# Optimization experiments

Hardware: AMD Instinct MI355X
Metric: run time of the kernel (lower is better)

## Reference

```python
import jax, jax.numpy as jnp
import numpy as np

INF = 1e20


def setup_inputs() -> dict:
    key = jax.random.key(0)
    k1, k2, k3 = jax.random.split(key, 3)
    B, Q, M, F, D = 16, 64, 512, 16, 512
    return {
        "query_embed": jax.random.normal(k1, (B, Q, D), dtype=jnp.float32),
        "in_memory_embed": jax.random.normal(k2, (B, M, F, D), dtype=jnp.float32),
        "out_memory_embed": jax.random.normal(k3, (B, M, F, D), dtype=jnp.float32),
        "ctx_mask": jnp.ones((B, M, F), dtype=jnp.float32),
        "query_mask": jnp.ones((B, Q), dtype=jnp.float32),
    }


def reference(query_embed, in_memory_embed, out_memory_embed, ctx_mask, query_mask):
    # co-attention scores: [B, Q, M, F]
    attention = jnp.einsum("bqd,bmfd->bqmf", query_embed, in_memory_embed)
    # additive INF masking (torch: mask*att - (1-mask)*INF)
    cm = ctx_mask[:, None, :, :]            # [B,1,M,F]
    attention = cm * attention - (1.0 - cm) * INF
    qm = query_mask[:, :, None, None]       # [B,Q,1,1]
    attention = qm * attention - (1.0 - qm) * INF
    # NOTE: torch code computes a max-pool over Q for kb_feature_att but
    # immediately overwrites it with softmax of a ones/ctx mask -> dead code.
    mask = ctx_mask * 1.0 - (1.0 - ctx_mask) * INF        # [B,M,F]
    kb_feature_att = jax.nn.softmax(mask, axis=-1)        # [B,M,F]
    # weighted read over feature slots: [B,M,D]
    in_mem = jnp.einsum("bmf,bmfd->bmd", kb_feature_att, in_memory_embed)
    out_mem = out_memory_embed.sum(axis=2)                # [B,M,D]
    # max-pool over feature axis F -> [B,Q,M]
    att_qm = attention.max(axis=-1)
    probs = jax.nn.softmax(att_qm, axis=-1)               # over M
    new_query_embed = query_embed + jnp.einsum("bqm,bmd->bqd", probs, out_mem)
    probs2 = jax.nn.softmax(att_qm, axis=1)               # over Q
    in_mem = in_mem + jnp.einsum("bqm,bqd->bmd", probs2, new_query_embed)
    return (new_query_embed, in_mem, out_mem)
```

## Files before the change

kernel.cpp:

```cpp
#include <hip/hip_runtime.h>

#define INF_F 1e20f
#define B_ 16
#define Q_ 64
#define M_ 512
#define F_ 16
#define D_ 512

typedef __attribute__((ext_vector_type(8))) short short8v;
typedef __attribute__((ext_vector_type(4))) float f32x4;

static __device__ __forceinline__ float bits_f(unsigned int u) { return __uint_as_float(u); }
static __device__ __forceinline__ float lo_f(unsigned int u) { return __uint_as_float(u << 16); }
static __device__ __forceinline__ float hi_f(unsigned int u) { return __uint_as_float(u & 0xffff0000u); }

static __device__ __forceinline__ int lds_off(int row, int gran) {
    return row * 40 + ((gran ^ (row & 3)) << 3);
}

static __device__ __forceinline__ void conv_store(short* __restrict__ Hb, short* __restrict__ Lb,
                                                  int row, int c, float4 v) {
    unsigned ux = __float_as_uint(v.x), uy = __float_as_uint(v.y);
    unsigned uz = __float_as_uint(v.z), uw = __float_as_uint(v.w);
    unsigned hx = ux & 0xffff0000u, hy = uy & 0xffff0000u;
    unsigned hz = uz & 0xffff0000u, hw = uw & 0xffff0000u;
    float lx = v.x - bits_f(hx), ly = v.y - bits_f(hy);
    float lz = v.z - bits_f(hz), lw = v.w - bits_f(hw);
    uint2 H, L;
    H.x = (hx >> 16) | hy;
    H.y = (hz >> 16) | hw;
    L.x = (__float_as_uint(lx) >> 16) | (__float_as_uint(ly) & 0xffff0000u);
    L.y = (__float_as_uint(lz) >> 16) | (__float_as_uint(lw) & 0xffff0000u);
    int off = row * 40 + (((c >> 1) ^ (row & 3)) << 3) + ((c & 1) << 2);
    *(uint2*)&Hb[off] = H;
    *(uint2*)&Lb[off] = L;
}

__global__ __launch_bounds__(256) void k_att_mfma(
    const float* __restrict__ query, const float* __restrict__ in_mem,
    const float* __restrict__ ctx_mask, const float* __restrict__ query_mask,
    float* __restrict__ att_qm, float* __restrict__ in_mem_base)
{
    __shared__ __align__(16) short Qh[2][64 * 40];
    __shared__ __align__(16) short Ql[2][64 * 40];
    __shared__ __align__(16) short Mh[2][64 * 40];
    __shared__ __align__(16) short Ml[2][64 * 40];

    const int bid = blockIdx.x;
    const int b   = bid & 15;
    const int m0  = (bid >> 4) * 4;
    const int t   = threadIdx.x;
    const int w   = t >> 6;
    const int lane = t & 63;
    const int lr  = lane & 15;
    const int lg  = lane >> 4;
    const int c8  = lane & 7;
    const int fg  = lane >> 3;

    float w_lo, w_hi;
    {
        const float* cm = ctx_mask + ((size_t)b * M_ + m0 + w) * F_;
        float wv[F_]; float mx = -INF_F;
        #pragma unroll
        for (int f = 0; f < F_; ++f) {
            float cv = cm[f];
            float v = cv - (1.0f - cv) * INF_F;
            wv[f] = v; mx = fmaxf(mx, v);
        }
        float s = 0.f;
        #pragma unroll
        for (int f = 0; f < F_; ++f) { wv[f] = __expf(wv[f] - mx); s += wv[f]; }
        float inv = 1.0f / s;
        w_lo = wv[fg] * inv; w_hi = wv[fg + 8] * inv;
    }

    const float4* q4 = (const float4*)query;
    const float4* m4 = (const float4*)in_mem;
    const size_t qbase = (size_t)b * Q_ * 128;
    const size_t mbase = ((size_t)b * M_ + m0) * F_ * 128;
    const int srow0 = t >> 3, scol = t & 7;
    const int srow1 = srow0 + 32;

    f32x4 acc[4];
    #pragma unroll
    for (int j = 0; j < 4; ++j) acc[j] = (f32x4){0, 0, 0, 0};

    float4 qA[2], mA[2], qB[2], mB[2];

#define LOAD_CHUNK(qd, md, kc) do { int k4 = (kc) * 8;                           \
        qd[0] = q4[qbase + (size_t)srow0 * 128 + k4 + scol];                     \
        qd[1] = q4[qbase + (size_t)srow1 * 128 + k4 + scol];                     \
        md[0] = m4[mbase + (size_t)srow0 * 128 + k4 + scol];                     \
        md[1] = m4[mbase + (size_t)srow1 * 128 + k4 + scol]; } while (0)

#define CONV_CHUNK(qd, md, bi) do {                                              \
        conv_store(Qh[bi], Ql[bi], srow0, scol, qd[0]);                          \
        conv_store(Qh[bi], Ql[bi], srow1, scol, qd[1]);                          \
        conv_store(Mh[bi], Ml[bi], srow0, scol, md[0]);                          \
        conv_store(Mh[bi], Ml[bi], srow1, scol, md[1]); } while (0)

#define MFMA_FSUM(bi, kc) do {                                                   \
        short8v bh = *(const short8v*)&Mh[bi][lds_off(w * 16 + lr, lg)];         \
        short8v bl = *(const short8v*)&Ml[bi][lds_off(w * 16 + lr, lg)];         \
        _Pragma("unroll")                                                        \
        for (int tq = 0; tq < 4; ++tq) {                                         \
            short8v ah = *(const short8v*)&Qh[bi][lds_off(tq * 16 + lr, lg)];    \
            short8v al = *(const short8v*)&Ql[bi][lds_off(tq * 16 + lr, lg)];    \
            acc[tq] = __builtin_amdgcn_mfma_f32_16x16x32_bf16(ah, bh, acc[tq], 0, 0, 0); \
            acc[tq] = __builtin_amdgcn_mfma_f32_16x16x32_bf16(ah, bl, acc[tq], 0, 0, 0); \
            acc[tq] = __builtin_amdgcn_mfma_f32_16x16x32_bf16(al, bh, acc[tq], 0, 0, 0); \
        }                                                                        \
        float4 s = make_float4(0, 0, 0, 0);                                      \
        {   int rr = w * 16 + fg;                                                \
            int off = rr * 40 + (((c8 >> 1) ^ (rr & 3)) << 3) + ((c8 & 1) << 2); \
            uint2 H = *(const uint2*)&Mh[bi][off];                               \
            uint2 L = *(const uint2*)&Ml[bi][off];                               \
            s.x += w_lo * (lo_f(H.x) + lo_f(L.x));                               \
            s.y += w_lo * (hi_f(H.x) + hi_f(L.x));                               \
            s.z += w_lo * (lo_f(H.y) + lo_f(L.y));                               \
            s.w += w_lo * (hi_f(H.y) + hi_f(L.y));                               \
        }                                                                        \
        {   int rr = w * 16 + fg + 8;                                            \
            int off = rr * 40 + (((c8 >> 1) ^ (rr & 3)) << 3) + ((c8 & 1) << 2); \
            uint2 H = *(const uint2*)&Mh[bi][off];                               \
            uint2 L = *(const uint2*)&Ml[bi][off];                               \
            s.x += w_hi * (lo_f(H.x) + lo_f(L.x));                               \
            s.y += w_hi * (hi_f(H.x) + hi_f(L.x));                               \
            s.z += w_hi * (lo_f(H.y) + lo_f(L.y));                               \
            s.w += w_hi * (hi_f(H.y) + hi_f(L.y));                               \
        }                                                                        \
        _Pragma("unroll")                                                        \
        for (int sh = 8; sh <= 32; sh <<= 1) {                                   \
            s.x += __shfl_xor(s.x, sh, 64); s.y += __shfl_xor(s.y, sh, 64);      \
            s.z += __shfl_xor(s.z, sh, 64); s.w += __shfl_xor(s.w, sh, 64);      \
        }                                                                        \
        if (fg == 0)                                                             \
            ((float4*)in_mem_base)[((size_t)b * M_ + m0 + w) * 128 + (kc) * 8 + c8] = s; \
    } while (0)

    LOAD_CHUNK(qA, mA, 0);
    #pragma unroll
    for (int it = 0; it < 8; ++it) {
        int kc0 = 2 * it, kc1 = 2 * it + 1;
        LOAD_CHUNK(qB, mB, kc1);
        CONV_CHUNK(qA, mA, 0);
        __syncthreads();
        MFMA_FSUM(0, kc0);
        if (it < 7) LOAD_CHUNK(qA, mA, kc0 + 2);
        CONV_CHUNK(qB, mB, 1);
        __syncthreads();
        MFMA_FSUM(1, kc1);
    }

    {
        int m = m0 + w;
        float cmv = ctx_mask[((size_t)b * M_ + m) * F_ + lr];
        #pragma unroll
        for (int tq = 0; tq < 4; ++tq) {
            #pragma unroll
            for (int rg = 0; rg < 4; ++rg) {
                int q = tq * 16 + lg * 4 + rg;
                float qmv = query_mask[b * Q_ + q];
                float v = acc[tq][rg];
                v = cmv * v - (1.0f - cmv) * INF_F;
                v = qmv * v - (1.0f - qmv) * INF_F;
                #pragma unroll
                for (int sh = 1; sh < 16; sh <<= 1) v = fmaxf(v, __shfl_xor(v, sh, 64));
                if (lr == 0)
                    att_qm[((size_t)b * Q_ + q) * M_ + m] = v;
            }
        }
    }
#undef LOAD_CHUNK
#undef CONV_CHUNK
#undef MFMA_FSUM
}

__global__ __launch_bounds__(256) void k_out_sum(
    const float* __restrict__ om, float* __restrict__ os)
{
    int bm = blockIdx.x * 2 + (threadIdx.x >> 7);
    int c  = threadIdx.x & 127;
    const float4* src = (const float4*)om + (size_t)bm * F_ * 128 + c;
    float4 a = make_float4(0, 0, 0, 0);
    #pragma unroll
    for (int f = 0; f < F_; ++f) {
        float4 v = src[(size_t)f * 128];
        a.x += v.x; a.y += v.y; a.z += v.z; a.w += v.w;
    }
    ((float4*)os)[(size_t)bm * 128 + c] = a;
}

__global__ __launch_bounds__(128) void k_new_query(
    const float* __restrict__ att, const float* __restrict__ query,
    const float* __restrict__ out_sum, float* __restrict__ new_q)
{
    __shared__ float P[8][512];
    int bid = blockIdx.x;
    int b = bid & 15, qc = bid >> 4;
    int t = threadIdx.x;
    {
        int qi = t >> 4, l16 = t & 15;
        const float* row = att + ((size_t)b * Q_ + qc * 8 + qi) * M_;
        float vals[32]; float mx = -INF_F;
        #pragma unroll
        for (int i = 0; i < 32; ++i) { vals[i] = row[l16 + i * 16]; mx = fmaxf(mx, vals[i]); }
        #pragma unroll
        for (int s = 1; s < 16; s <<= 1) mx = fmaxf(mx, __shfl_xor(mx, s, 64));
        float sm = 0.f;
        #pragma unroll
        for (int i = 0; i < 32; ++i) { vals[i] = __expf(vals[i] - mx); sm += vals[i]; }
        #pragma unroll
        for (int s = 1; s < 16; s <<= 1) sm += __shfl_xor(sm, s, 64);
        float inv = 1.0f / sm;
        #pragma unroll
        for (int i = 0; i < 32; ++i) P[qi][l16 + i * 16] = vals[i] * inv;
    }
    __syncthreads();
    int c = t;
    const float4* o4 = (const float4*)out_sum + (size_t)b * M_ * 128 + c;
    const float4* q4 = (const float4*)query + ((size_t)b * Q_ + qc * 8) * 128 + c;
    float4 acc[8];
    #pragma unroll
    for (int qi = 0; qi < 8; ++qi) acc[qi] = q4[(size_t)qi * 128];
    for (int mm = 0; mm < M_; mm += 4) {
        float4 o0 = o4[(size_t)(mm + 0) * 128];
        float4 o1 = o4[(size_t)(mm + 1) * 128];
        float4 o2 = o4[(size_t)(mm + 2) * 128];
        float4 o3 = o4[(size_t)(mm + 3) * 128];
        #pragma unroll
        for (int qi = 0; qi < 8; ++qi) {
            float4 p = *(const float4*)&P[qi][mm];
            acc[qi].x += p.x * o0.x + p.y * o1.x + p.z * o2.x + p.w * o3.x;
            acc[qi].y += p.x * o0.y + p.y * o1.y + p.z * o2.y + p.w * o3.y;
            acc[qi].z += p.x * o0.z + p.y * o1.z + p.z * o2.z + p.w * o3.z;
            acc[qi].w += p.x * o0.w + p.y * o1.w + p.z * o2.w + p.w * o3.w;
        }
    }
    float4* n4 = (float4*)new_q + ((size_t)b * Q_ + qc * 8) * 128 + c;
    #pragma unroll
    for (int qi = 0; qi < 8; ++qi) n4[(size_t)qi * 128] = acc[qi];
}

__global__ __launch_bounds__(128) void k_in_mem(
    const float* __restrict__ att, const float* __restrict__ new_q,
    float* __restrict__ in_mem_io)
{
    __shared__ float P[8][64];
    int bid = blockIdx.x;
    int b = bid & 15, mc = bid >> 4;
    int m0 = mc * 8;
    int t = threadIdx.x;
    {
        int mi = t >> 4, l16 = t & 15;
        float v[4]; float mx = -INF_F;
        #pragma unroll
        for (int i = 0; i < 4; ++i) {
            v[i] = att[((size_t)b * Q_ + l16 + i * 16) * M_ + m0 + mi];
            mx = fmaxf(mx, v[i]);
        }
        #pragma unroll
        for (int s = 1; s < 16; s <<= 1) mx = fmaxf(mx, __shfl_xor(mx, s, 64));
        float sm = 0.f;
        #pragma unroll
        for (int i = 0; i < 4; ++i) { v[i] = __expf(v[i] - mx); sm += v[i]; }
        #pragma unroll
        for (int s = 1; s < 16; s <<= 1) sm += __shfl_xor(sm, s, 64);
        float inv = 1.0f / sm;
        #pragma unroll
        for (int i = 0; i < 4; ++i) P[mi][l16 + i * 16] = v[i] * inv;
    }
    __syncthreads();
    int c = t;
    float4* io = (float4*)in_mem_io + ((size_t)b * M_ + m0) * 128 + c;
    const float4* n4 = (const float4*)new_q + (size_t)b * Q_ * 128 + c;
    float4 acc[8];
    #pragma unroll
    for (int mi = 0; mi < 8; ++mi) acc[mi] = io[(size_t)mi * 128];
    for (int q = 0; q < Q_; q += 4) {
        float4 n0 = n4[(size_t)(q + 0) * 128];
        float4 n1 = n4[(size_t)(q + 1) * 128];
        float4 n2 = n4[(size_t)(q + 2) * 128];
        float4 n3 = n4[(size_t)(q + 3) * 128];
        #pragma unroll
        for (int mi = 0; mi < 8; ++mi) {
            float4 p = *(const float4*)&P[mi][q];
            acc[mi].x += p.x * n0.x + p.y * n1.x + p.z * n2.x + p.w * n3.x;
            acc[mi].y += p.x * n0.y + p.y * n1.y + p.z * n2.y + p.w * n3.y;
            acc[mi].z += p.x * n0.z + p.y * n1.z + p.z * n2.z + p.w * n3.z;
            acc[mi].w += p.x * n0.w + p.y * n1.w + p.z * n2.w + p.w * n3.w;
        }
    }
    #pragma unroll
    for (int mi = 0; mi < 8; ++mi) io[(size_t)mi * 128] = acc[mi];
}

extern "C" void kernel_launch(void* const* d_in, const int* in_sizes, int n_in,
                              void* d_out, int out_size, void* d_ws, size_t ws_size,
                              hipStream_t stream)
{
    const float* query      = (const float*)d_in[0];
    const float* in_mem     = (const float*)d_in[1];
    const float* out_mem    = (const float*)d_in[2];
    const float* ctx_mask   = (const float*)d_in[3];
    const float* query_mask = (const float*)d_in[4];

    float* out = (float*)d_out;
    float* new_q      = out;
    float* in_mem_out = out + (size_t)B_*Q_*D_;
    float* out_mem_o  = in_mem_out + (size_t)B_*M_*D_;

    float* att_qm = (float*)d_ws;

    hipLaunchKernelGGL(k_att_mfma, dim3((M_/4) * B_), dim3(256), 0, stream,
                       query, in_mem, ctx_mask, query_mask, att_qm, in_mem_out);
    hipLaunchKernelGGL(k_out_sum, dim3(B_*M_/2), dim3(256), 0, stream,
                       out_mem, out_mem_o);
    hipLaunchKernelGGL(k_new_query, dim3(8 * B_), dim3(128), 0, stream,
                       att_qm, query, out_mem_o, new_q);
    hipLaunchKernelGGL(k_in_mem, dim3(64 * B_), dim3(128), 0, stream,
                       att_qm, new_q, in_mem_out);
}
```

Measured before the change: 229.6 us.

## Fuse out-memory feature sum into attention kernel and pre-split query to bf16

The separate out_memory feature-sum kernel is folded into the main MFMA attention kernel, which now streams out_mem alongside in_mem and reduces over F with warp shuffles. The query is split into bf16 hi/lo once by a new pre-pass kernel, so each attention block no longer reconverts it and just copies the pre-split halves into LDS. The weighted in_mem read now uses the fp32 values held in registers instead of rereading the split values from LDS, and __syncthreads is replaced by an explicit lgkmcnt wait plus s_barrier. The fused kernel carries more register pressure and a larger per-block load, and there is one extra small launch.

After: 238.0 us. 1.04x slower.

```diff
diff --git a/kernel.cpp b/kernel.cpp
--- a/kernel.cpp
+++ b/kernel.cpp
@@ -11,40 +11,54 @@
 typedef __attribute__((ext_vector_type(4))) float f32x4;
 
 static __device__ __forceinline__ float bits_f(unsigned int u) { return __uint_as_float(u); }
-static __device__ __forceinline__ float lo_f(unsigned int u) { return __uint_as_float(u << 16); }
-static __device__ __forceinline__ float hi_f(unsigned int u) { return __uint_as_float(u & 0xffff0000u); }
 
 static __device__ __forceinline__ int lds_off(int row, int gran) {
     return row * 40 + ((gran ^ (row & 3)) << 3);
 }
 
+static __device__ __forceinline__ void split4(float4 v, uint2& H, uint2& L) {
+    unsigned hx = __float_as_uint(v.x) & 0xffff0000u, hy = __float_as_uint(v.y) & 0xffff0000u;
+    unsigned hz = __float_as_uint(v.z) & 0xffff0000u, hw = __float_as_uint(v.w) & 0xffff0000u;
+    H.x = (hx >> 16) | hy;
+    H.y = (hz >> 16) | hw;
+    L.x = (__float_as_uint(v.x - bits_f(hx)) >> 16) | (__float_as_uint(v.y - bits_f(hy)) & 0xffff0000u);
+    L.y = (__float_as_uint(v.z - bits_f(hz)) >> 16) | (__float_as_uint(v.w - bits_f(hw)) & 0xffff0000u);
+}
+
 static __device__ __forceinline__ void conv_store(short* __restrict__ Hb, short* __restrict__ Lb,
                                                   int row, int c, float4 v) {
-    unsigned ux = __float_as_uint(v.x), uy = __float_as_uint(v.y);
-    unsigned uz = __float_as_uint(v.z), uw = __float_as_uint(v.w);
-    unsigned hx = ux & 0xffff0000u, hy = uy & 0xffff0000u;
-    unsigned hz = uz & 0xffff0000u, hw = uw & 0xffff0000u;
-    float lx = v.x - bits_f(hx), ly = v.y - bits_f(hy);
-    float lz = v.z - bits_f(hz), lw = v.w - bits_f(hw);
     uint2 H, L;
-    H.x = (hx >> 16) | hy;
-    H.y = (hz >> 16) | hw;
-    L.x = (__float_as_uint(lx) >> 16) | (__float_as_uint(ly) & 0xffff0000u);
-    L.y = (__float_as_uint(lz) >> 16) | (__float_as_uint(lw) & 0xffff0000u);
+    split4(v, H, L);
     int off = row * 40 + (((c >> 1) ^ (row & 3)) << 3) + ((c & 1) << 2);
     *(uint2*)&Hb[off] = H;
     *(uint2*)&Lb[off] = L;
 }
 
+__global__ __launch_bounds__(256) void k_q_split(
+    const float* __restrict__ q, uint2* __restrict__ qh, uint2* __restrict__ ql)
+{
+    int fid = blockIdx.x * 256 + threadIdx.x;
+    float4 v = ((const float4*)q)[fid];
+    int col = fid & 127, row = (fid >> 7) & 63, b = fid >> 13;
+    int kc = col >> 3, sub = col & 7;
+    uint2 H, L;
+    split4(v, H, L);
+    size_t oidx = ((size_t)(b * 16 + kc) * 512) + row * 8 + sub;
+    qh[oidx] = H;
+    ql[oidx] = L;
+}
+
 __global__ __launch_bounds__(256) void k_att_mfma(
-    const float* __restrict__ query, const float* __restrict__ in_mem,
+    const uint2* __restrict__ qhg, const uint2* __restrict__ qlg,
+    const float* __restrict__ in_mem, const float* __restrict__ out_mem,
     const float* __restrict__ ctx_mask, const float* __restrict__ query_mask,
-    float* __restrict__ att_qm, float* __restrict__ in_mem_base)
-{
-    __shared__ __align__(16) short Qh[2][64 * 40];
-    __shared__ __align__(16) short Ql[2][64 * 40];
-    __shared__ __align__(16) short Mh[2][64 * 40];
-    __shared__ __align__(16) short Ml[2][64 * 40];
+    float* __restrict__ att_qm, float* __restrict__ in_mem_base,
+    float* __restrict__ out_mem_sum)
+{
+    __shared__ __align__(16) short Qh[2][2560];
+    __shared__ __align__(16) short Ql[2][2560];
+    __shared__ __align__(16) short Mh[2][2560];
+    __shared__ __align__(16) short Ml[2][2560];
 
     const int bid = blockIdx.x;
     const int b   = bid & 15;
@@ -54,10 +68,11 @@
     const int lane = t & 63;
     const int lr  = lane & 15;
     const int lg  = lane >> 4;
-    const int c8  = lane & 7;
-    const int fg  = lane >> 3;
-
-    float w_lo, w_hi;
+    const int r0  = (t >> 3) * 2, r1 = r0 + 1;
+    const int scol = t & 7;
+    const int f0  = r0 & 15, f1 = f0 + 1;
+
+    float w0, w1;
     {
         const float* cm = ctx_mask + ((size_t)b * M_ + m0 + w) * F_;
         float wv[F_]; float mx = -INF_F;
@@ -71,85 +86,86 @@
         #pragma unroll
         for (int f = 0; f < F_; ++f) { wv[f] = __expf(wv[f] - mx); s += wv[f]; }
         float inv = 1.0f / s;
-        w_lo = wv[fg] * inv; w_hi = wv[fg + 8] * inv;
-    }
-
-    const float4* q4 = (const float4*)query;
+        w0 = wv[f0] * inv; w1 = wv[f1] * inv;
+    }
+
     const float4* m4 = (const float4*)in_mem;
-    const size_t qbase = (size_t)b * Q_ * 128;
+    const float4* o4 = (const float4*)out_mem;
     const size_t mbase = ((size_t)b * M_ + m0) * F_ * 128;
-    const int srow0 = t >> 3, scol = t & 7;
-    const int srow1 = srow0 + 32;
+    const size_t qimg  = (size_t)b * 16 * 512;
 
     f32x4 acc[4];
     #pragma unroll
     for (int j = 0; j < 4; ++j) acc[j] = (f32x4){0, 0, 0, 0};
 
-    float4 qA[2], mA[2], qB[2], mB[2];
-
-#define LOAD_CHUNK(qd, md, kc) do { int k4 = (kc) * 8;                           \
-        qd[0] = q4[qbase + (size_t)srow0 * 128 + k4 + scol];                     \
-        qd[1] = q4[qbase + (size_t)srow1 * 128 + k4 + scol];                     \
-        md[0] = m4[mbase + (size_t)srow0 * 128 + k4 + scol];                     \
-        md[1] = m4[mbase + (size_t)srow1 * 128 + k4 + scol]; } while (0)
-
-#define CONV_CHUNK(qd, md, bi) do {                                              \
-        conv_store(Qh[bi], Ql[bi], srow0, scol, qd[0]);                          \
-        conv_store(Qh[bi], Ql[bi], srow1, scol, qd[1]);                          \
-        conv_store(Mh[bi], Ml[bi], srow0, scol, md[0]);                          \
-        conv_store(Mh[bi], Ml[bi], srow1, scol, md[1]); } while (0)
-
-#define MFMA_FSUM(bi, kc) do {                                                   \
-        short8v bh = *(const short8v*)&Mh[bi][lds_off(w * 16 + lr, lg)];         \
-        short8v bl = *(const short8v*)&Ml[bi][lds_off(w * 16 + lr, lg)];         \
-        _Pragma("unroll")                                                        \
-        for (int tq = 0; tq < 4; ++tq) {                                         \
-            short8v ah = *(const short8v*)&Qh[bi][lds_off(tq * 16 + lr, lg)];    \
-            short8v al = *(const short8v*)&Ql[bi][lds_off(tq * 16 + lr, lg)];    \
+    uint2 qhA[2], qlA[2], qhB[2], qlB[2];
+    float4 mA[2], oA[2], mB[2], oB[2];
+
+#define LOAD_CHUNK(qh_, ql_, m_, o_, kc) do { int k4 = (kc) * 8;               \
+        qh_[0] = qhg[qimg + (size_t)(kc) * 512 + t];                           \
+        qh_[1] = qhg[qimg + (size_t)(kc) * 512 + t + 256];                     \
+        ql_[0] = qlg[qimg + (size_t)(kc) * 512 + t];                           \
+        ql_[1] = qlg[qimg + (size_t)(kc) * 512 + t + 256];                     \
+        m_[0] = m4[mbase + (size_t)r0 * 128 + k4 + scol];                      \
+        m_[1] = m4[mbase + (size_t)r1 * 128 + k4 + scol];                      \
+        o_[0] = o4[mbase + (size_t)r0 * 128 + k4 + scol];                      \
+        o_[1] = o4[mbase + (size_t)r1 * 128 + k4 + scol]; } while (0)
+
+#define CONV(qh_, ql_, m_, bi) do {                                            \
+        _Pragma("unroll")                                                      \
+        for (int i = 0; i < 2; ++i) {                                          \
+            int idx = t + i * 256, row = idx >> 3, sub = idx & 7;              \
+            int off = row * 40 + (((sub >> 1) ^ (row & 3)) << 3) + ((sub & 1) << 2); \
+            *(uint2*)&Qh[bi][off] = qh_[i];                                    \
+            *(uint2*)&Ql[bi][off] = ql_[i];                                    \
+        }                                                                      \
+        conv_store(Mh[bi], Ml[bi], r0, scol, m_[0]);                           \
+        conv_store(Mh[bi], Ml[bi], r1, scol, m_[1]); } while (0)
+
+#define BARRIER() do { asm volatile("s_waitcnt lgkmcnt(0)" ::: "memory");      \
+        __builtin_amdgcn_s_barrier(); } while (0)
+
+#define MFMA_RED(bi, m_, o_, kc) do {                                          \
+        short8v bh = *(const short8v*)&Mh[bi][lds_off(w * 16 + lr, lg)];       \
+        short8v bl = *(const short8v*)&Ml[bi][lds_off(w * 16 + lr, lg)];       \
+        _Pragma("unroll")                                                      \
+        for (int tq = 0; tq < 4; ++tq) {                                       \
+            short8v ah = *(const short8v*)&Qh[bi][lds_off(tq * 16 + lr, lg)];  \
+            short8v al = *(const short8v*)&Ql[bi][lds_off(tq * 16 + lr, lg)];  \
             acc[tq] = __builtin_amdgcn_mfma_f32_16x16x32_bf16(ah, bh, acc[tq], 0, 0, 0); \
             acc[tq] = __builtin_amdgcn_mfma_f32_16x16x32_bf16(ah, bl, acc[tq], 0, 0, 0); \
             acc[tq] = __builtin_amdgcn_mfma_f32_16x16x32_bf16(al, bh, acc[tq], 0, 0, 0); \
-        }                                                                        \
-        float4 s = make_float4(0, 0, 0, 0);                                      \
-        {   int rr = w * 16 + fg;                                                \
-            int off = rr * 40 + (((c8 >> 1) ^ (rr & 3)) << 3) + ((c8 & 1) << 2); \
-            uint2 H = *(const uint2*)&Mh[bi][off];                               \
-            uint2 L = *(const uint2*)&Ml[bi][off];                               \
-            s.x += w_lo * (lo_f(H.x) + lo_f(L.x));                               \
-            s.y += w_lo * (hi_f(H.x) + hi_f(L.x));                               \
-            s.z += w_lo * (lo_f(H.y) + lo_f(L.y));                               \
-            s.w += w_lo * (hi_f(H.y) + hi_f(L.y));                               \
-        }                                                                        \
-        {   int rr = w * 16 + fg + 8;                                            \
-            int off = rr * 40 + (((c8 >> 1) ^ (rr & 3)) << 3) + ((c8 & 1) << 2); \
-            uint2 H = *(const uint2*)&Mh[bi][off];                               \
-            uint2 L = *(const uint2*)&Ml[bi][off];                               \
-            s.x += w_hi * (lo_f(H.x) + lo_f(L.x));                               \
-            s.y += w_hi * (hi_f(H.x) + hi_f(L.x));                               \
-            s.z += w_hi * (lo_f(H.y) + lo_f(L.y));                               \
-            s.w += w_hi * (hi_f(H.y) + hi_f(L.y));                               \
-        }                                                                        \
-        _Pragma("unroll")                                                        \
-        for (int sh = 8; sh <= 32; sh <<= 1) {                                   \
-            s.x += __shfl_xor(s.x, sh, 64); s.y += __shfl_xor(s.y, sh, 64);      \
-            s.z += __shfl_xor(s.z, sh, 64); s.w += __shfl_xor(s.w, sh, 64);      \
-        }                                                                        \
-        if (fg == 0)                                                             \
-            ((float4*)in_mem_base)[((size_t)b * M_ + m0 + w) * 128 + (kc) * 8 + c8] = s; \
-    } while (0)
-
-    LOAD_CHUNK(qA, mA, 0);
+        }                                                                      \
+        float4 pin, pout;                                                      \
+        pin.x = w0 * m_[0].x + w1 * m_[1].x;  pin.y = w0 * m_[0].y + w1 * m_[1].y; \
+        pin.z = w0 * m_[0].z + w1 * m_[1].z;  pin.w = w0 * m_[0].w + w1 * m_[1].w; \
+        pout.x = o_[0].x + o_[1].x;  pout.y = o_[0].y + o_[1].y;               \
+        pout.z = o_[0].z + o_[1].z;  pout.w = o_[0].w + o_[1].w;               \
+        _Pragma("unroll")                                                      \
+        for (int sh = 8; sh <= 32; sh <<= 1) {                                 \
+            pin.x += __shfl_xor(pin.x, sh, 64);  pin.y += __shfl_xor(pin.y, sh, 64);  \
+            pin.z += __shfl_xor(pin.z, sh, 64);  pin.w += __shfl_xor(pin.w, sh, 64);  \
+            pout.x += __shfl_xor(pout.x, sh, 64); pout.y += __shfl_xor(pout.y, sh, 64); \
+            pout.z += __shfl_xor(pout.z, sh, 64); pout.w += __shfl_xor(pout.w, sh, 64); \
+        }                                                                      \
+        if (lane < 8) {                                                        \
+            size_t oi = ((size_t)b * M_ + m0 + w) * 128 + (kc) * 8 + lane;     \
+            ((float4*)in_mem_base)[oi] = pin;                                  \
+            ((float4*)out_mem_sum)[oi] = pout;                                 \
+        } } while (0)
+
+    LOAD_CHUNK(qhA, qlA, mA, oA, 0);
     #pragma unroll
     for (int it = 0; it < 8; ++it) {
         int kc0 = 2 * it, kc1 = 2 * it + 1;
-        LOAD_CHUNK(qB, mB, kc1);
-        CONV_CHUNK(qA, mA, 0);
-        __syncthreads();
-        MFMA_FSUM(0, kc0);
-        if (it < 7) LOAD_CHUNK(qA, mA, kc0 + 2);
-        CONV_CHUNK(qB, mB, 1);
-        __syncthreads();
-        MFMA_FSUM(1, kc1);
+        LOAD_CHUNK(qhB, qlB, mB, oB, kc1);
+        CONV(qhA, qlA, mA, 0);
+        BARRIER();
+        MFMA_RED(0, mA, oA, kc0);
+        if (it < 7) LOAD_CHUNK(qhA, qlA, mA, oA, kc0 + 2);
+        CONV(qhB, qlB, mB, 1);
+        BARRIER();
+        MFMA_RED(1, mB, oB, kc1);
     }
 
     {
@@ -172,23 +188,9 @@
         }
     }
 #undef LOAD_CHUNK
-#undef CONV_CHUNK
-#undef MFMA_FSUM
-}
-
-__global__ __launch_bounds__(256) void k_out_sum(
-    const float* __restrict__ om, float* __restrict__ os)
-{
-    int bm = blockIdx.x * 2 + (threadIdx.x >> 7);
-    int c  = threadIdx.x & 127;
-    const float4* src = (const float4*)om + (size_t)bm * F_ * 128 + c;
-    float4 a = make_float4(0, 0, 0, 0);
-    #pragma unroll
-    for (int f = 0; f < F_; ++f) {
-        float4 v = src[(size_t)f * 128];
-        a.x += v.x; a.y += v.y; a.z += v.z; a.w += v.w;
-    }
-    ((float4*)os)[(size_t)bm * 128 + c] = a;
+#undef CONV
+#undef BARRIER
+#undef MFMA_RED
 }
 
 __global__ __launch_bounds__(128) void k_new_query(
@@ -310,12 +312,16 @@
     float* in_mem_out = out + (size_t)B_*Q_*D_;
     float* out_mem_o  = in_mem_out + (size_t)B_*M_*D_;
 
-    float* att_qm = (float*)d_ws;
-
+    float* ws     = (float*)d_ws;
+    float* att_qm = ws;
+    uint2* qh     = (uint2*)(ws + (size_t)B_*Q_*M_);
+    uint2* ql     = qh + (size_t)B_*16*512;
+
+    hipLaunchKernelGGL(k_q_split, dim3(B_*Q_*128/256), dim3(256), 0, stream,
+                       query, qh, ql);
     hipLaunchKernelGGL(k_att_mfma, dim3((M_/4) * B_), dim3(256), 0, stream,
-                       query, in_mem, ctx_mask, query_mask, att_qm, in_mem_out);
-    hipLaunchKernelGGL(k_out_sum, dim3(B_*M_/2), dim3(256), 0, stream,
-                       out_mem, out_mem_o);
+                       qh, ql, in_mem, out_mem, ctx_mask, query_mask,
+                       att_qm, in_mem_out, out_mem_o);
     hipLaunchKernelGGL(k_new_query, dim3(8 * B_), dim3(128), 0, stream,
                        att_qm, query, out_mem_o, new_q);
     hipLaunchKernelGGL(k_in_mem, dim3(64 * B_), dim3(128), 0, stream,
```
